# Optimization experiments

Measured on AMD Instinct MI355X. Metric: run time of the kernel, lower is better.

Reference implementation:

```python
import jax, jax.numpy as jnp
import numpy as np

B, N, C, D, K = 8, 4096, 64, 64, 16


def _knn_indices(features, k):
    # so topk-smallest indices match torch.cdist + topk(largest=False))
    sq = jnp.sum(features * features, axis=-1)                      # [B, N]
    d2 = sq[:, :, None] + sq[:, None, :] - 2.0 * jnp.einsum('bic,bjc->bij', features, features)
    n = features.shape[1]
    eye = jnp.eye(n, dtype=bool)[None]                              # mask self
    d2 = jnp.where(eye, jnp.inf, d2)
    _, idx = jax.lax.top_k(-d2, k)                                  # k smallest
    return idx                                                      # [B, N, k]


def setup_inputs() -> dict:
    key = jax.random.key(0)
    k0, k1, k2 = jax.random.split(key, 3)
    features = jax.random.normal(k0, (B, N, C), dtype=jnp.float32)
    W1 = jax.random.normal(k1, (2 * C, D), dtype=jnp.float32) * 0.05
    b1 = jnp.zeros((D,), dtype=jnp.float32)
    W2 = jax.random.normal(k2, (D, D), dtype=jnp.float32) * 0.05
    b2 = jnp.zeros((D,), dtype=jnp.float32)
    return {"features": features, "W1": W1, "b1": b1, "W2": W2, "b2": b2}


def reference(features, W1, b1, W2, b2):
    idx = _knn_indices(features, K)                                 # [B, N, K]
    neighbors = jax.vmap(lambda f, i: f[i])(features, idx)          # [B, N, K, C]
    central = features[:, :, None, :]                               # [B, N, 1, C]
    edge = jnp.concatenate(
        [jnp.broadcast_to(central, neighbors.shape), neighbors - central], axis=-1
    )                                                               # [B, N, K, 2C]
    h = jax.nn.gelu(edge @ W1 + b1, approximate=False)              # exact GELU (torch default)
    h = jax.nn.gelu(h @ W2 + b2, approximate=False)                 # [B, N, K, D]
    return jnp.max(h, axis=2)                                       # [B, N, D]
```

## Files before the change

kernel.cpp:

```cpp
#include <hip/hip_runtime.h>
#include <math.h>
#include <stdint.h>

#define B 8
#define N 4096
#define C 64
#define D 64
#define K 16

typedef __attribute__((ext_vector_type(8))) short short8;
typedef __attribute__((ext_vector_type(4))) float f32x4;

__device__ __forceinline__ unsigned short f2bf(float x) {
    unsigned u = __float_as_uint(x);
    unsigned r = (u + 0x7FFFu + ((u >> 16) & 1u)) >> 16;
    return (unsigned short)r;
}
__device__ __forceinline__ float bf2f(unsigned short h) {
    return __uint_as_float(((unsigned)h) << 16);
}

__device__ __forceinline__ double pack_key(float d2, unsigned idx) {
    uint2 u; u.x = idx; u.y = __float_as_uint(d2);
    return __builtin_bit_cast(double, u);
}

__global__ __launch_bounds__(256)
void prep_kernel(const float* __restrict__ F, float* __restrict__ sq,
                 unsigned short* __restrict__ HP, unsigned short* __restrict__ MP,
                 unsigned short* __restrict__ LP) {
    const int row = blockIdx.x * 256 + threadIdx.x;
    const float4* src = (const float4*)(F + (size_t)row * C);
    float4 v[16];
    #pragma unroll
    for (int q = 0; q < 16; q++) v[q] = src[q];

    {
        float r[8];
        #pragma unroll
        for (int j = 0; j < 8; j++) {
            float t = ((const float*)v)[j];
            r[j] = t * t;
        }
        #pragma unroll
        for (int m = 1; m < 8; m++) {
            #pragma unroll
            for (int j = 0; j < 8; j++) {
                float t = ((const float*)v)[8 * m + j];
                r[j] = fmaf(t, t, r[j]);
            }
        }
        sq[row] = ((r[0] + r[1]) + (r[2] + r[3])) + ((r[4] + r[5]) + (r[6] + r[7]));
    }

    uint4* dh = (uint4*)(HP + (size_t)row * C);
    uint4* dm = (uint4*)(MP + (size_t)row * C);
    uint4* dl = (uint4*)(LP + (size_t)row * C);
    #pragma unroll
    for (int c8 = 0; c8 < 8; c8++) {
        unsigned hq[4], mq[4], lq[4];
        #pragma unroll
        for (int e = 0; e < 4; e++) {
            float x0 = ((const float*)v)[c8 * 8 + 2 * e];
            float x1 = ((const float*)v)[c8 * 8 + 2 * e + 1];
            unsigned short h0 = f2bf(x0), h1 = f2bf(x1);
            float r10 = x0 - bf2f(h0), r11 = x1 - bf2f(h1);
            unsigned short m0 = f2bf(r10), m1 = f2bf(r11);
            float r20 = r10 - bf2f(m0), r21 = r11 - bf2f(m1);
            unsigned short l0 = f2bf(r20), l1 = f2bf(r21);
            hq[e] = (unsigned)h0 | ((unsigned)h1 << 16);
            mq[e] = (unsigned)m0 | ((unsigned)m1 << 16);
            lq[e] = (unsigned)l0 | ((unsigned)l1 << 16);
        }
        dh[c8] = make_uint4(hq[0], hq[1], hq[2], hq[3]);
        dm[c8] = make_uint4(mq[0], mq[1], mq[2], mq[3]);
        dl[c8] = make_uint4(lq[0], lq[1], lq[2], lq[3]);
    }
}

__device__ __forceinline__ void merge4_store(const uint64_t* __restrict__ keys,
                                             int qloc, uint64_t* __restrict__ dst) {
    const uint64_t* K0 = keys + (qloc * 4 + 0) * 16;
    const uint64_t* K1 = keys + (qloc * 4 + 1) * 16;
    const uint64_t* K2 = keys + (qloc * 4 + 2) * 16;
    const uint64_t* K3 = keys + (qloc * 4 + 3) * 16;
    int p0 = 0, p1 = 0, p2 = 0, p3 = 0;
    uint64_t h0 = K0[0], h1 = K1[0], h2 = K2[0], h3 = K3[0];
    #pragma unroll
    for (int k = 0; k < K; k++) {
        uint64_t m01 = h0 < h1 ? h0 : h1;
        uint64_t m23 = h2 < h3 ? h2 : h3;
        uint64_t mv  = m01 < m23 ? m01 : m23;
        dst[k] = mv;
        if      (mv == h0) { ++p0; h0 = (p0 < 16) ? K0[p0] : ~0ull; }
        else if (mv == h1) { ++p1; h1 = (p1 < 16) ? K1[p1] : ~0ull; }
        else if (mv == h2) { ++p2; h2 = (p2 < 16) ? K2[p2] : ~0ull; }
        else               { ++p3; h3 = (p3 < 16) ? K3[p3] : ~0ull; }
    }
}

__global__ __launch_bounds__(512, 2)
void knn_mfma_kernel(const unsigned short* __restrict__ HP,
                     const unsigned short* __restrict__ MP,
                     const unsigned short* __restrict__ LP,
                     const float* __restrict__ sqg, uint64_t* __restrict__ keysg) {
    __shared__ __align__(16) char lds[49152];

    const int s  = blockIdx.y;
    const int b  = blockIdx.z;
    const int i0 = blockIdx.x * 128;
    const int c0 = s * 2048;
    const unsigned short* Hb = HP + (size_t)b * N * C;
    const unsigned short* Mb = MP + (size_t)b * N * C;
    const unsigned short* Lb = LP + (size_t)b * N * C;
    const float* sqb = sqg + (size_t)b * N;

    const int tid = threadIdx.x;
    const int l   = tid & 63;
    const int w   = tid >> 6;

    const int lr  = tid >> 3;
    const int lq  = tid & 7;
    const int wbyte = (lr * 128 + lq * 16) ^ ((lr & 7) << 4);

    const double KMAX = __builtin_bit_cast(double, 0x7FEFFFFFFFFFFFFFull);

    uint4 ph, pm, pl;
    {
        const size_t rb = (size_t)(c0 + lr) * C + lq * 8;
        ph = *(const uint4*)(Hb + rb);
        pm = *(const uint4*)(Mb + rb);
        pl = *(const uint4*)(Lb + rb);
    }

    {
        const size_t r0 = (size_t)(i0 + lr) * C + lq * 8;
        const size_t r1 = (size_t)(i0 + 64 + lr) * C + lq * 8;
        uint4 qh0 = *(const uint4*)(Hb + r0), qh1 = *(const uint4*)(Hb + r1);
        uint4 qm0 = *(const uint4*)(Mb + r0), qm1 = *(const uint4*)(Mb + r1);
        uint4 ql0 = *(const uint4*)(Lb + r0), ql1 = *(const uint4*)(Lb + r1);
        *(uint4*)(lds +              wbyte) = qh0;
        *(uint4*)(lds +  8192      + wbyte) = qm0;
        *(uint4*)(lds + 16384      + wbyte) = ql0;
        *(uint4*)(lds + 24576      + wbyte) = qh1;
        *(uint4*)(lds + 24576+8192 + wbyte) = qm1;
        *(uint4*)(lds + 24576+16384+ wbyte) = ql1;
    }
    __syncthreads();

    const int koff = (l >> 4) * 16;
    const int swzR = (l & 7) << 4;
    const int qrow = w * 16 + (l & 15);
    const char* qbuf = lds + ((qrow >> 6) ? 24576 : 0);
    const int qr6 = qrow & 63;
    const int qb0 = (qr6 * 128 + koff) ^ swzR;
    const int qb1 = (qr6 * 128 + 64 + koff) ^ swzR;
    short8 bh0 = *(const short8*)(qbuf + qb0),         bh1 = *(const short8*)(qbuf + qb1);
    short8 bm0 = *(const short8*)(qbuf +  8192 + qb0), bm1 = *(const short8*)(qbuf +  8192 + qb1);
    short8 bl0 = *(const short8*)(qbuf + 16384 + qb0), bl1 = *(const short8*)(qbuf + 16384 + qb1);

    const float sqq   = sqb[i0 + qrow];
    const int   qglob = i0 + qrow;
    const int   crow0 = (l >> 4) * 4;
    const int   dtile = i0 + ((w >> 2) << 6);

    __syncthreads();

    *(uint4*)(lds +         wbyte) = ph;
    *(uint4*)(lds +  8192 + wbyte) = pm;
    *(uint4*)(lds + 16384 + wbyte) = pl;
    {
        const size_t rb = (size_t)(c0 + 64 + lr) * C + lq * 8;
        ph = *(const uint4*)(Hb + rb);
        pm = *(const uint4*)(Mb + rb);
        pl = *(const uint4*)(Lb + rb);
    }
    __syncthreads();

    double bd[16];
    #pragma unroll
    for (int k = 0; k < 16; k++) bd[k] = KMAX;

    for (int t = 0; t < 32; t++) {
        const int j0 = c0 + t * 64;
        char* bufA = lds + ((t & 1) ? 24576 : 0);
        char* bufB = lds + ((t & 1) ? 0 : 24576);

        if (t < 31) {
            *(uint4*)(bufB +         wbyte) = ph;
            *(uint4*)(bufB +  8192 + wbyte) = pm;
            *(uint4*)(bufB + 16384 + wbyte) = pl;
        }
        if (t < 30) {
            const size_t rb = (size_t)(j0 + 128 + lr) * C + lq * 8;
            ph = *(const uint4*)(Hb + rb);
            pm = *(const uint4*)(Mb + rb);
            pl = *(const uint4*)(Lb + rb);
        }

        float4 sqm0 = *(const float4*)(sqb + j0 +      crow0);
        float4 sqm1 = *(const float4*)(sqb + j0 + 16 + crow0);
        float4 sqm2 = *(const float4*)(sqb + j0 + 32 + crow0);
        float4 sqm3 = *(const float4*)(sqb + j0 + 48 + crow0);

        double nk[16];

        #pragma unroll
        for (int m = 0; m < 4; m++) {
            const int arow = m * 16 + (l & 15);
            const int ab0 = (arow * 128 + koff) ^ swzR;
            const int ab1 = (arow * 128 + 64 + koff) ^ swzR;
            short8 ah0 = *(const short8*)(bufA + ab0);
            short8 ah1 = *(const short8*)(bufA + ab1);
            short8 am0 = *(const short8*)(bufA + 8192 + ab0);
            short8 am1 = *(const short8*)(bufA + 8192 + ab1);
            short8 al0 = *(const short8*)(bufA + 16384 + ab0);
            short8 al1 = *(const short8*)(bufA + 16384 + ab1);

            f32x4 acc1 = {0.f, 0.f, 0.f, 0.f};
            acc1 = __builtin_amdgcn_mfma_f32_16x16x32_bf16(am0, bm0, acc1, 0, 0, 0);
            acc1 = __builtin_amdgcn_mfma_f32_16x16x32_bf16(am1, bm1, acc1, 0, 0, 0);
            acc1 = __builtin_amdgcn_mfma_f32_16x16x32_bf16(ah0, bl0, acc1, 0, 0, 0);
            acc1 = __builtin_amdgcn_mfma_f32_16x16x32_bf16(ah1, bl1, acc1, 0, 0, 0);
            acc1 = __builtin_amdgcn_mfma_f32_16x16x32_bf16(al0, bh0, acc1, 0, 0, 0);
            f32x4 acc2 = {0.f, 0.f, 0.f, 0.f};
            acc2 = __builtin_amdgcn_mfma_f32_16x16x32_bf16(al1, bh1, acc2, 0, 0, 0);
            acc2 = __builtin_amdgcn_mfma_f32_16x16x32_bf16(ah0, bm0, acc2, 0, 0, 0);
            acc2 = __builtin_amdgcn_mfma_f32_16x16x32_bf16(ah1, bm1, acc2, 0, 0, 0);
            acc2 = __builtin_amdgcn_mfma_f32_16x16x32_bf16(am0, bh0, acc2, 0, 0, 0);
            acc2 = __builtin_amdgcn_mfma_f32_16x16x32_bf16(am1, bh1, acc2, 0, 0, 0);
            f32x4 acch = {0.f, 0.f, 0.f, 0.f};
            acch = __builtin_amdgcn_mfma_f32_16x16x32_bf16(ah0, bh0, acch, 0, 0, 0);
            acch = __builtin_amdgcn_mfma_f32_16x16x32_bf16(ah1, bh1, acch, 0, 0, 0);

            float4 sqm = (m == 0) ? sqm0 : (m == 1) ? sqm1 : (m == 2) ? sqm2 : sqm3;
            #pragma unroll
            for (int r = 0; r < 4; r++) {
                float sqc = (r == 0) ? sqm.x : (r == 1) ? sqm.y : (r == 2) ? sqm.z : sqm.w;
                float gg = acch[r] + (acc1[r] + acc2[r]);
                float d2 = fmaf(-2.0f, gg, sqq + sqc);
                d2 = fmaxf(d2, 0.0f);
                nk[m * 4 + r] = pack_key(d2, (unsigned)(j0 + m * 16 + crow0 + r));
            }
        }

        if (j0 == dtile) {
            #pragma unroll
            for (int m = 0; m < 4; m++)
                #pragma unroll
                for (int r = 0; r < 4; r++)
                    if ((j0 + m * 16 + crow0 + r) == qglob) nk[m * 4 + r] = KMAX;
        }

        #pragma unroll
        for (int p = 1; p < 16; p <<= 1) {
            #pragma unroll
            for (int kk = p; kk >= 1; kk >>= 1) {
                #pragma unroll
                for (int j = kk % p; j <= 16 - 1 - kk; j += 2 * kk) {
                    #pragma unroll
                    for (int i = 0; i <= ((kk - 1 < 16 - j - kk - 1) ? kk - 1 : 16 - j - kk - 1); i++) {
                        if ((i + j) / (2 * p) == (i + j + kk) / (2 * p)) {
                            double a = nk[i + j], c2 = nk[i + j + kk];
                            nk[i + j]      = fmax(a, c2);
                            nk[i + j + kk] = fmin(a, c2);
                        }
                    }
                }
            }
        }
        #pragma unroll
        for (int i = 0; i < 16; i++) bd[i] = fmin(bd[i], nk[i]);
        #pragma unroll
        for (int j = 8; j > 0; j >>= 1) {
            #pragma unroll
            for (int i = 0; i < 16; i++) {
                int ixj = i ^ j;
                if (ixj > i) {
                    double a = bd[i], c2 = bd[ixj];
                    bd[i]   = fmin(a, c2);
                    bd[ixj] = fmax(a, c2);
                }
            }
        }

        __syncthreads();
    }

    uint64_t* keys = (uint64_t*)lds;
    if (w < 4) {
        const int qloc = w * 16 + (l & 15);
        const int base = (qloc * 4 + (l >> 4)) * 16;
        #pragma unroll
        for (int k = 0; k < 16; k++)
            keys[base + k] = __builtin_bit_cast(uint64_t, bd[k]);
    }
    __syncthreads();
    if (tid < 64)
        merge4_store(keys, tid, keysg + ((size_t)b * N + i0 + tid) * 32 + s * 16);
    __syncthreads();
    if (w >= 4) {
        const int qloc = (w - 4) * 16 + (l & 15);
        const int base = (qloc * 4 + (l >> 4)) * 16;
        #pragma unroll
        for (int k = 0; k < 16; k++)
            keys[base + k] = __builtin_bit_cast(uint64_t, bd[k]);
    }
    __syncthreads();
    if (tid < 64)
        merge4_store(keys, tid, keysg + ((size_t)b * N + i0 + 64 + tid) * 32 + s * 16);
}

__global__ __launch_bounds__(256)
void knn_merge_kernel(const uint64_t* __restrict__ keysg, int* __restrict__ knn) {
    const int q = blockIdx.x * 256 + threadIdx.x;
    const uint64_t* A  = keysg + (size_t)q * 32;
    const uint64_t* Bp = A + 16;
    int pa = 0, pb = 0;
    uint64_t ha = A[0], hb = Bp[0];
    int* dst = knn + (size_t)q * K;
    #pragma unroll
    for (int k = 0; k < K; k++) {
        uint64_t mv = ha < hb ? ha : hb;
        dst[k] = (int)(mv & 0xFFFFFFFFu);
        if (mv == ha) { ++pa; ha = (pa < 16) ? A[pa] : ~0ull; }
        else          { ++pb; hb = (pb < 16) ? Bp[pb] : ~0ull; }
    }
}

__device__ __forceinline__ float gelu_fast(float x) {
    float az = fabsf(x) * 0.70710678118654752440f;
    float t  = __builtin_amdgcn_rcpf(fmaf(0.3275911f, az, 1.0f));
    float p  = t * fmaf(t, fmaf(t, fmaf(t, fmaf(t, 1.061405429f, -1.453152027f),
                                        1.421413741f), -0.284496736f), 0.254829592f);
    float e  = p * __builtin_amdgcn_exp2f(-az * az * 1.44269504088896f);
    float g  = 0.5f * x;
    return (x >= 0.0f) ? g * (2.0f - e) : g * e;
}

#define QPW 4

__global__ __launch_bounds__(256)
void mlp_mfma_kernel(const float* __restrict__ F,
                     const unsigned short* __restrict__ HP,
                     const unsigned short* __restrict__ MP,
                     const int* __restrict__ knn,
                     const float* __restrict__ W1, const float* __restrict__ b1,
                     const float* __restrict__ W2, const float* __restrict__ b2,
                     float* __restrict__ out) {
    __shared__ __align__(16) unsigned short W1h[64 * 128];
    __shared__ __align__(16) unsigned short W1m[64 * 128];
    __shared__ __align__(16) unsigned short hbh[4][1024];
    __shared__ __align__(16) unsigned short hbm[4][1024];

    const int tid = threadIdx.x;
    const int l   = tid & 63;
    const int w   = tid >> 6;

    const int cb   = (l >> 4) * 8;
    const int swzL = (l & 15) << 4;
    const int qbase = (blockIdx.x * 4 + w) * QPW;

    int nbs[QPW];
    #pragma unroll
    for (int jq = 0; jq < QPW; jq++)
        nbs[jq] = knn[(size_t)(qbase + jq) * K + (l & 15)];

    for (int e = tid; e < 8192; e += 256) {
        const int n = e & 63, k = e >> 6;
        const int srcrow = (k < 64) ? (64 + k) : (k - 64);
        float x = W1[srcrow * 64 + n];
        unsigned short hh = f2bf(x);
        unsigned short mm = f2bf(x - bf2f(hh));
        const int byte = (n * 256 + k * 2) ^ ((n & 15) << 4);
        *(unsigned short*)((char*)W1h + byte) = hh;
        *(unsigned short*)((char*)W1m + byte) = mm;
    }

    short8 B2h[4][2], B2m[4][2];
    float b1v[4], b2v[4];
    {
        const int n = (l & 15);
        #pragma unroll
        for (int nt = 0; nt < 4; nt++) {
            const int nn = nt * 16 + n;
            b1v[nt] = b1[nn];
            b2v[nt] = b2[nn];
            #pragma unroll
            for (int c = 0; c < 2; c++) {
                const int k0 = c * 32 + (l >> 4) * 8;
                short8 vh, vm;
                #pragma unroll
                for (int jj = 0; jj < 8; jj++) {
                    float x = W2[(k0 + jj) * 64 + nn];
                    unsigned short hh = f2bf(x);
                    vh[jj] = (short)hh;
                    vm[jj] = (short)f2bf(x - bf2f(hh));
                }
                B2h[nt][c] = vh; B2m[nt][c] = vm;
            }
        }
    }
    __syncthreads();

    float4 pnA0[2], pnA1[2], pnB0[2], pnB1[2];
    #define LOADN(s_, jq_) { \
        const int q_ = qbase + (jq_); \
        const float* Fb_ = F + (size_t)(q_ >> 12) * N * C; \
        const size_t nr_ = (size_t)nbs[jq_] * C; \
        pnA0[s_] = *(const float4*)(Fb_ + nr_ + cb); \
        pnA1[s_] = *(const float4*)(Fb_ + nr_ + cb + 4); \
        pnB0[s_] = *(const float4*)(Fb_ + nr_ + 32 + cb); \
        pnB1[s_] = *(const float4*)(Fb_ + nr_ + 36 + cb); \
    }
    LOADN(0, 0);

    #pragma unroll
    for (int jq = 0; jq < QPW; jq++) {
        const int sbuf = jq & 1;
        if (jq + 1 < QPW) LOADN(sbuf ^ 1, jq + 1);

        const int q  = qbase + jq;
        const int b  = q >> 12;
        const int ci = q & (N - 1);
        const float*          Fb  = F  + (size_t)b * N * C;
        const unsigned short* HPb = HP + (size_t)b * N * C;
        const unsigned short* MPb = MP + (size_t)b * N * C;

        float4 cA0 = *(const float4*)(Fb + (size_t)ci * C + cb);
        float4 cA1 = *(const float4*)(Fb + (size_t)ci * C + cb + 4);
        float4 cB0 = *(const float4*)(Fb + (size_t)ci * C + 32 + cb);
        float4 cB1 = *(const float4*)(Fb + (size_t)ci * C + 36 + cb);
        float4 nA0 = pnA0[sbuf], nA1 = pnA1[sbuf];
        float4 nB0 = pnB0[sbuf], nB1 = pnB1[sbuf];

        short8 ach0 = *(const short8*)(HPb + (size_t)ci * C + cb);
        short8 ach1 = *(const short8*)(HPb + (size_t)ci * C + 32 + cb);
        short8 acm0 = *(const short8*)(MPb + (size_t)ci * C + cb);
        short8 acm1 = *(const short8*)(MPb + (size_t)ci * C + 32 + cb);

        short8 adh0, adm0, adh1, adm1;
        {
            float d0[8] = {nA0.x - cA0.x, nA0.y - cA0.y, nA0.z - cA0.z, nA0.w - cA0.w,
                           nA1.x - cA1.x, nA1.y - cA1.y, nA1.z - cA1.z, nA1.w - cA1.w};
            float d1[8] = {nB0.x - cB0.x, nB0.y - cB0.y, nB0.z - cB0.z, nB0.w - cB0.w,
                           nB1.x - cB1.x, nB1.y - cB1.y, nB1.z - cB1.z, nB1.w - cB1.w};
            #pragma unroll
            for (int jj = 0; jj < 8; jj++) {
                unsigned short h0 = f2bf(d0[jj]);
                adh0[jj] = (short)h0; adm0[jj] = (short)f2bf(d0[jj] - bf2f(h0));
                unsigned short h1 = f2bf(d1[jj]);
                adh1[jj] = (short)h1; adm1[jj] = (short)f2bf(d1[jj] - bf2f(h1));
            }
        }

        #pragma unroll
        for (int nt = 0; nt < 4; nt++) {
            const int rowb = (nt * 16 + (l & 15)) * 256 + (l >> 4) * 16;
            f32x4 a1 = {0.f, 0.f, 0.f, 0.f};
            f32x4 a2 = {0.f, 0.f, 0.f, 0.f};
            #pragma unroll
            for (int kc = 0; kc < 4; kc++) {
                const int byte = (rowb + kc * 64) ^ swzL;
                short8 Bh = *(const short8*)((char*)W1h + byte);
                short8 Bm = *(const short8*)((char*)W1m + byte);
                short8 Ah = (kc == 0) ? adh0 : (kc == 1) ? adh1 : (kc == 2) ? ach0 : ach1;
                short8 Am = (kc == 0) ? adm0 : (kc == 1) ? adm1 : (kc == 2) ? acm0 : acm1;
                a1 = __builtin_amdgcn_mfma_f32_16x16x32_bf16(Ah, Bh, a1, 0, 0, 0);
                a2 = __builtin_amdgcn_mfma_f32_16x16x32_bf16(Ah, Bm, a2, 0, 0, 0);
                a2 = __builtin_amdgcn_mfma_f32_16x16x32_bf16(Am, Bh, a2, 0, 0, 0);
            }
            #pragma unroll
            for (int r = 0; r < 4; r++) {
                const int row = (l >> 4) * 4 + r;
                const int col = nt * 16 + (l & 15);
                float hv = gelu_fast(a1[r] + a2[r] + b1v[nt]);
                unsigned short hh = f2bf(hv);
                unsigned short hm = f2bf(hv - bf2f(hh));
                const int byte = (row * 128 + col * 2) ^ ((row & 7) << 4);
                *(unsigned short*)((char*)&hbh[w][0] + byte) = hh;
                *(unsigned short*)((char*)&hbm[w][0] + byte) = hm;
            }
        }

        asm volatile("s_waitcnt lgkmcnt(0)" ::: "memory");
        __builtin_amdgcn_sched_barrier(0);

        short8 Ah2[2], Am2[2];
        #pragma unroll
        for (int kc = 0; kc < 2; kc++) {
            const int byte = ((l & 15) * 128 + kc * 64 + (l >> 4) * 16) ^ (((l & 15) & 7) << 4);
            Ah2[kc] = *(const short8*)((char*)&hbh[w][0] + byte);
            Am2[kc] = *(const short8*)((char*)&hbm[w][0] + byte);
        }
        #pragma unroll
        for (int nt = 0; nt < 4; nt++) {
            f32x4 a1 = {0.f, 0.f, 0.f, 0.f};
            f32x4 a2 = {0.f, 0.f, 0.f, 0.f};
            #pragma unroll
            for (int kc = 0; kc < 2; kc++) {
                a1 = __builtin_amdgcn_mfma_f32_16x16x32_bf16(Ah2[kc], B2h[nt][kc], a1, 0, 0, 0);
                a2 = __builtin_amdgcn_mfma_f32_16x16x32_bf16(Ah2[kc], B2m[nt][kc], a2, 0, 0, 0);
                a2 = __builtin_amdgcn_mfma_f32_16x16x32_bf16(Am2[kc], B2h[nt][kc], a2, 0, 0, 0);
            }
            float mx = -INFINITY;
            #pragma unroll
            for (int r = 0; r < 4; r++)
                mx = fmaxf(mx, gelu_fast(a1[r] + a2[r] + b2v[nt]));
            mx = fmaxf(mx, __shfl_xor(mx, 16));
            mx = fmaxf(mx, __shfl_xor(mx, 32));
            if (l < 16) out[(size_t)q * D + nt * 16 + l] = mx;
        }
    }
    #undef LOADN
}

extern "C" void kernel_launch(void* const* d_in, const int* in_sizes, int n_in,
                              void* d_out, int out_size, void* d_ws, size_t ws_size,
                              hipStream_t stream) {
    const float* F  = (const float*)d_in[0];
    const float* W1 = (const float*)d_in[1];
    const float* b1 = (const float*)d_in[2];
    const float* W2 = (const float*)d_in[3];
    const float* b2 = (const float*)d_in[4];
    float* out = (float*)d_out;

    char* ws = (char*)d_ws;
    float*          sq   = (float*)ws;
    uint64_t*       keys = (uint64_t*)(ws + (128 << 10));
    unsigned short* HP   = (unsigned short*)(ws + (8320 << 10));
    unsigned short* MP   = (unsigned short*)(ws + (12416 << 10));
    unsigned short* LP   = (unsigned short*)(ws + (16512 << 10));
    int*            knn  = (int*)LP;

    prep_kernel<<<dim3(B * N / 256), 256, 0, stream>>>(F, sq, HP, MP, LP);
    knn_mfma_kernel<<<dim3(N / 128, 2, B), 512, 0, stream>>>(HP, MP, LP, sq, keys);
    knn_merge_kernel<<<dim3(B * N / 256), 256, 0, stream>>>(keys, knn);
    mlp_mfma_kernel<<<dim3(B * N / (4 * QPW)), 256, 0, stream>>>(
        F, HP, MP, knn, W1, b1, W2, b2, out);
}
```

Before: 267.9 us.

## Precompute split-bf16 weights in prep kernel and software-pipeline MLP layers

The bf16 hi/lo splitting and swizzling of W1 and W2 moves into one block of the prep kernel. Each MLP block now copies the ready-made weights into LDS with vector loads instead of converting them itself, which removes repeated per-block conversion work across 2048 blocks. The MLP loop is also restructured so that layer 1 of the next query is issued before layer 2 of the current one, to overlap MFMA, LDS and global-load latency. In exchange, the single-block weight prep adds a serial tail to the prep kernel and the pipelined loop uses more registers.

```diff
diff --git a/kernel.cpp b/kernel.cpp
--- a/kernel.cpp
+++ b/kernel.cpp
@@ -28,7 +28,10 @@
 __global__ __launch_bounds__(256)
 void prep_kernel(const float* __restrict__ F, float* __restrict__ sq,
                  unsigned short* __restrict__ HP, unsigned short* __restrict__ MP,
-                 unsigned short* __restrict__ LP) {
+                 unsigned short* __restrict__ LP,
+                 const float* __restrict__ W1, const float* __restrict__ W2,
+                 unsigned short* __restrict__ W1hg, unsigned short* __restrict__ W1mg,
+                 unsigned short* __restrict__ W2Th, unsigned short* __restrict__ W2Tm) {
     const int row = blockIdx.x * 256 + threadIdx.x;
     const float4* src = (const float4*)(F + (size_t)row * C);
     float4 v[16];
@@ -75,6 +78,27 @@
         dh[c8] = make_uint4(hq[0], hq[1], hq[2], hq[3]);
         dm[c8] = make_uint4(mq[0], mq[1], mq[2], mq[3]);
         dl[c8] = make_uint4(lq[0], lq[1], lq[2], lq[3]);
+    }
+
+    if (blockIdx.x == 0) {
+        const int tid = threadIdx.x;
+        for (int e = tid; e < 8192; e += 256) {
+            const int n = e & 63, k = e >> 6;
+            const int srcrow = (k < 64) ? (64 + k) : (k - 64);
+            float x = W1[srcrow * 64 + n];
+            unsigned short hh = f2bf(x);
+            unsigned short mm = f2bf(x - bf2f(hh));
+            const int byte = (n * 256 + k * 2) ^ ((n & 15) << 4);
+            *(unsigned short*)((char*)W1hg + byte) = hh;
+            *(unsigned short*)((char*)W1mg + byte) = mm;
+        }
+        for (int e = tid; e < 4096; e += 256) {
+            const int n = e & 63, k = e >> 6;
+            float x = W2[k * 64 + n];
+            unsigned short hh = f2bf(x);
+            W2Th[n * 64 + k] = hh;
+            W2Tm[n * 64 + k] = f2bf(x - bf2f(hh));
+        }
     }
 }
 
@@ -345,8 +369,11 @@
                      const unsigned short* __restrict__ HP,
                      const unsigned short* __restrict__ MP,
                      const int* __restrict__ knn,
-                     const float* __restrict__ W1, const float* __restrict__ b1,
-                     const float* __restrict__ W2, const float* __restrict__ b2,
+                     const unsigned short* __restrict__ W1hg,
+                     const unsigned short* __restrict__ W1mg,
+                     const unsigned short* __restrict__ W2Th,
+                     const unsigned short* __restrict__ W2Tm,
+                     const float* __restrict__ b1, const float* __restrict__ b2,
                      float* __restrict__ out) {
     __shared__ __align__(16) unsigned short W1h[64 * 128];
     __shared__ __align__(16) unsigned short W1m[64 * 128];
@@ -357,54 +384,50 @@
     const int l   = tid & 63;
     const int w   = tid >> 6;
 
-    const int cb   = (l >> 4) * 8;
-    const int swzL = (l & 15) << 4;
+    const int cb    = (l >> 4) * 8;
+    const int swzL  = (l & 15) << 4;
     const int qbase = (blockIdx.x * 4 + w) * QPW;
+    char* hbh_w = (char*)&hbh[w][0];
+    char* hbm_w = (char*)&hbm[w][0];
 
     int nbs[QPW];
     #pragma unroll
     for (int jq = 0; jq < QPW; jq++)
         nbs[jq] = knn[(size_t)(qbase + jq) * K + (l & 15)];
 
-    for (int e = tid; e < 8192; e += 256) {
-        const int n = e & 63, k = e >> 6;
-        const int srcrow = (k < 64) ? (64 + k) : (k - 64);
-        float x = W1[srcrow * 64 + n];
-        unsigned short hh = f2bf(x);
-        unsigned short mm = f2bf(x - bf2f(hh));
-        const int byte = (n * 256 + k * 2) ^ ((n & 15) << 4);
-        *(unsigned short*)((char*)W1h + byte) = hh;
-        *(unsigned short*)((char*)W1m + byte) = mm;
+    {
+        const uint4* s1 = (const uint4*)W1hg;
+        const uint4* s2 = (const uint4*)W1mg;
+        uint4* d1 = (uint4*)W1h;
+        uint4* d2 = (uint4*)W1m;
+        #pragma unroll
+        for (int i = 0; i < 4; i++) {
+            d1[tid + 256 * i] = s1[tid + 256 * i];
+            d2[tid + 256 * i] = s2[tid + 256 * i];
+        }
     }
 
     short8 B2h[4][2], B2m[4][2];
-    float b1v[4], b2v[4];
+    float4 b1v, b2v;
     {
         const int n = (l & 15);
+        b1v = make_float4(b1[n], b1[16 + n], b1[32 + n], b1[48 + n]);
+        b2v = make_float4(b2[n], b2[16 + n], b2[32 + n], b2[48 + n]);
         #pragma unroll
         for (int nt = 0; nt < 4; nt++) {
             const int nn = nt * 16 + n;
-            b1v[nt] = b1[nn];
-            b2v[nt] = b2[nn];
             #pragma unroll
             for (int c = 0; c < 2; c++) {
                 const int k0 = c * 32 + (l >> 4) * 8;
-                short8 vh, vm;
-                #pragma unroll
-                for (int jj = 0; jj < 8; jj++) {
-                    float x = W2[(k0 + jj) * 64 + nn];
-                    unsigned short hh = f2bf(x);
-                    vh[jj] = (short)hh;
-                    vm[jj] = (short)f2bf(x - bf2f(hh));
-                }
-                B2h[nt][c] = vh; B2m[nt][c] = vm;
+                B2h[nt][c] = *(const short8*)(W2Th + nn * 64 + k0);
+                B2m[nt][c] = *(const short8*)(W2Tm + nn * 64 + k0);
             }
         }
     }
     __syncthreads();
 
     float4 pnA0[2], pnA1[2], pnB0[2], pnB1[2];
-    #define LOADN(s_, jq_) { \
+#define LOADN(s_, jq_) { \
         const int q_ = qbase + (jq_); \
         const float* Fb_ = F + (size_t)(q_ >> 12) * N * C; \
         const size_t nr_ = (size_t)nbs[jq_] * C; \
@@ -413,106 +436,125 @@
         pnB0[s_] = *(const float4*)(Fb_ + nr_ + 32 + cb); \
         pnB1[s_] = *(const float4*)(Fb_ + nr_ + 36 + cb); \
     }
+
+#define MLP_L1(jq_) { \
+        const int q_  = qbase + (jq_); \
+        const int b_  = q_ >> 12; \
+        const int ci_ = q_ & (N - 1); \
+        const float*          Fb_  = F  + (size_t)b_ * N * C; \
+        const unsigned short* HPb_ = HP + (size_t)b_ * N * C; \
+        const unsigned short* MPb_ = MP + (size_t)b_ * N * C; \
+        float4 cA0 = *(const float4*)(Fb_ + (size_t)ci_ * C + cb); \
+        float4 cA1 = *(const float4*)(Fb_ + (size_t)ci_ * C + cb + 4); \
+        float4 cB0 = *(const float4*)(Fb_ + (size_t)ci_ * C + 32 + cb); \
+        float4 cB1 = *(const float4*)(Fb_ + (size_t)ci_ * C + 36 + cb); \
+        float4 nA0 = pnA0[(jq_) & 1], nA1 = pnA1[(jq_) & 1]; \
+        float4 nB0 = pnB0[(jq_) & 1], nB1 = pnB1[(jq_) & 1]; \
+        short8 ach0 = *(const short8*)(HPb_ + (size_t)ci_ * C + cb); \
+        short8 ach1 = *(const short8*)(HPb_ + (size_t)ci_ * C + 32 + cb); \
+        short8 acm0 = *(const short8*)(MPb_ + (size_t)ci_ * C + cb); \
+        short8 acm1 = *(const short8*)(MPb_ + (size_t)ci_ * C + 32 + cb); \
+        short8 adh0, adm0, adh1, adm1; \
+        { \
+            float d0[8] = {nA0.x-cA0.x, nA0.y-cA0.y, nA0.z-cA0.z, nA0.w-cA0.w, \
+                           nA1.x-cA1.x, nA1.y-cA1.y, nA1.z-cA1.z, nA1.w-cA1.w}; \
+            float d1[8] = {nB0.x-cB0.x, nB0.y-cB0.y, nB0.z-cB0.z, nB0.w-cB0.w, \
+                           nB1.x-cB1.x, nB1.y-cB1.y, nB1.z-cB1.z, nB1.w-cB1.w}; \
+            _Pragma("unroll") \
+            for (int jj = 0; jj < 8; jj++) { \
+                unsigned short h0_ = f2bf(d0[jj]); \
+                adh0[jj] = (short)h0_; adm0[jj] = (short)f2bf(d0[jj] - bf2f(h0_)); \
+                unsigned short h1_ = f2bf(d1[jj]); \
+                adh1[jj] = (short)h1_; adm1[jj] = (short)f2bf(d1[jj] - bf2f(h1_)); \
+            } \
+        } \
+        _Pragma("unroll") \
+        for (int nt = 0; nt < 4; nt++) { \
+            const int rowb = (nt * 16 + (l & 15)) * 256 + (l >> 4) * 16; \
+            f32x4 a1 = {0.f,0.f,0.f,0.f}; \
+            f32x4 a2 = {0.f,0.f,0.f,0.f}; \
+            _Pragma("unroll") \
+            for (int kc = 0; kc < 4; kc++) { \
+                const int byte_ = (rowb + kc * 64) ^ swzL; \
+                short8 Bh = *(const short8*)((char*)W1h + byte_); \
+                short8 Bm = *(const short8*)((char*)W1m + byte_); \
+                short8 Ah = (kc==0)?adh0:(kc==1)?adh1:(kc==2)?ach0:ach1; \
+                short8 Am = (kc==0)?adm0:(kc==1)?adm1:(kc==2)?acm0:acm1; \
+                a1 = __builtin_amdgcn_mfma_f32_16x16x32_bf16(Ah, Bh, a1, 0, 0, 0); \
+                a2 = __builtin_amdgcn_mfma_f32_16x16x32_bf16(Ah, Bm, a2, 0, 0, 0); \
+                a2 = __builtin_amdgcn_mfma_f32_16x16x32_bf16(Am, Bh, a2, 0, 0, 0); \
+            } \
+            float bnt = (nt==0)?b1v.x:(nt==1)?b1v.y:(nt==2)?b1v.z:b1v.w; \
+            _Pragma("unroll") \
+            for (int r = 0; r < 4; r++) { \
+                const int row = (l >> 4) * 4 + r; \
+                const int col = nt * 16 + (l & 15); \
+                float hv = gelu_fast(a1[r] + a2[r] + bnt); \
+                unsigned short hh_ = f2bf(hv); \
+                unsigned short hm_ = f2bf(hv - bf2f(hh_)); \
+                const int byte_ = (row * 128 + col * 2) ^ ((row & 7) << 4); \
+                *(unsigned short*)(hbh_w + byte_) = hh_; \
+                *(unsigned short*)(hbm_w + byte_) = hm_; \
+            } \
+        } \
+    }
+
+#define WAITREAD() { \
+        asm volatile("s_waitcnt lgkmcnt(0)" ::: "memory"); \
+        __builtin_amdgcn_sched_barrier(0); \
+        _Pragma("unroll") \
+        for (int kc = 0; kc < 2; kc++) { \
+            const int byte_ = ((l & 15) * 128 + kc * 64 + (l >> 4) * 16) ^ (((l & 15) & 7) << 4); \
+            A2h[kc] = *(const short8*)(hbh_w + byte_); \
+            A2m[kc] = *(const short8*)(hbm_w + byte_); \
+        } \
+    }
+
+#define MLP_L2(jq_) { \
+        const int q_ = qbase + (jq_); \
+        _Pragma("unroll") \
+        for (int nt = 0; nt < 4; nt++) { \
+            f32x4 a1 = {0.f,0.f,0.f,0.f}; \
+            f32x4 a2 = {0.f,0.f,0.f,0.f}; \
+            _Pragma("unroll") \
+            for (int kc = 0; kc < 2; kc++) { \
+                a1 = __builtin_amdgcn_mfma_f32_16x16x32_bf16(A2h[kc], B2h[nt][kc], a1, 0, 0, 0); \
+                a2 = __builtin_amdgcn_mfma_f32_16x16x32_bf16(A2h[kc], B2m[nt][kc], a2, 0, 0, 0); \
+                a2 = __builtin_amdgcn_mfma_f32_16x16x32_bf16(A2m[kc], B2h[nt][kc], a2, 0, 0, 0); \
+            } \
+            float bnt = (nt==0)?b2v.x:(nt==1)?b2v.y:(nt==2)?b2v.z:b2v.w; \
+            float mx = -INFINITY; \
+            _Pragma("unroll") \
+            for (int r = 0; r < 4; r++) \
+                mx = fmaxf(mx, gelu_fast(a1[r] + a2[r] + bnt)); \
+            mx = fmaxf(mx, __shfl_xor(mx, 16)); \
+            mx = fmaxf(mx, __shfl_xor(mx, 32)); \
+            if (l < 16) out[(size_t)q_ * D + nt * 16 + l] = mx; \
+        } \
+    }
+
+    short8 A2h[2], A2m[2];
+
     LOADN(0, 0);
+    LOADN(1, 1);
+    MLP_L1(0);
+    WAITREAD();
 
     #pragma unroll
     for (int jq = 0; jq < QPW; jq++) {
-        const int sbuf = jq & 1;
-        if (jq + 1 < QPW) LOADN(sbuf ^ 1, jq + 1);
-
-        const int q  = qbase + jq;
-        const int b  = q >> 12;
-        const int ci = q & (N - 1);
-        const float*          Fb  = F  + (size_t)b * N * C;
-        const unsigned short* HPb = HP + (size_t)b * N * C;
-        const unsigned short* MPb = MP + (size_t)b * N * C;
-
-        float4 cA0 = *(const float4*)(Fb + (size_t)ci * C + cb);
-        float4 cA1 = *(const float4*)(Fb + (size_t)ci * C + cb + 4);
-        float4 cB0 = *(const float4*)(Fb + (size_t)ci * C + 32 + cb);
-        float4 cB1 = *(const float4*)(Fb + (size_t)ci * C + 36 + cb);
-        float4 nA0 = pnA0[sbuf], nA1 = pnA1[sbuf];
-        float4 nB0 = pnB0[sbuf], nB1 = pnB1[sbuf];
-
-        short8 ach0 = *(const short8*)(HPb + (size_t)ci * C + cb);
-        short8 ach1 = *(const short8*)(HPb + (size_t)ci * C + 32 + cb);
-        short8 acm0 = *(const short8*)(MPb + (size_t)ci * C + cb);
-        short8 acm1 = *(const short8*)(MPb + (size_t)ci * C + 32 + cb);
-
-        short8 adh0, adm0, adh1, adm1;
-        {
-            float d0[8] = {nA0.x - cA0.x, nA0.y - cA0.y, nA0.z - cA0.z, nA0.w - cA0.w,
-                           nA1.x - cA1.x, nA1.y - cA1.y, nA1.z - cA1.z, nA1.w - cA1.w};
-            float d1[8] = {nB0.x - cB0.x, nB0.y - cB0.y, nB0.z - cB0.z, nB0.w - cB0.w,
-                           nB1.x - cB1.x, nB1.y - cB1.y, nB1.z - cB1.z, nB1.w - cB1.w};
-            #pragma unroll
-            for (int jj = 0; jj < 8; jj++) {
-                unsigned short h0 = f2bf(d0[jj]);
-                adh0[jj] = (short)h0; adm0[jj] = (short)f2bf(d0[jj] - bf2f(h0));
-                unsigned short h1 = f2bf(d1[jj]);
-                adh1[jj] = (short)h1; adm1[jj] = (short)f2bf(d1[jj] - bf2f(h1));
-            }
-        }
-
-        #pragma unroll
-        for (int nt = 0; nt < 4; nt++) {
-            const int rowb = (nt * 16 + (l & 15)) * 256 + (l >> 4) * 16;
-            f32x4 a1 = {0.f, 0.f, 0.f, 0.f};
-            f32x4 a2 = {0.f, 0.f, 0.f, 0.f};
-            #pragma unroll
-            for (int kc = 0; kc < 4; kc++) {
-                const int byte = (rowb + kc * 64) ^ swzL;
-                short8 Bh = *(const short8*)((char*)W1h + byte);
-                short8 Bm = *(const short8*)((char*)W1m + byte);
-                short8 Ah = (kc == 0) ? adh0 : (kc == 1) ? adh1 : (kc == 2) ? ach0 : ach1;
-                short8 Am = (kc == 0) ? adm0 : (kc == 1) ? adm1 : (kc == 2) ? acm0 : acm1;
-                a1 = __builtin_amdgcn_mfma_f32_16x16x32_bf16(Ah, Bh, a1, 0, 0, 0);
-                a2 = __builtin_amdgcn_mfma_f32_16x16x32_bf16(Ah, Bm, a2, 0, 0, 0);
-                a2 = __builtin_amdgcn_mfma_f32_16x16x32_bf16(Am, Bh, a2, 0, 0, 0);
-            }
-            #pragma unroll
-            for (int r = 0; r < 4; r++) {
-                const int row = (l >> 4) * 4 + r;
-                const int col = nt * 16 + (l & 15);
-                float hv = gelu_fast(a1[r] + a2[r] + b1v[nt]);
-                unsigned short hh = f2bf(hv);
-                unsigned short hm = f2bf(hv - bf2f(hh));
-                const int byte = (row * 128 + col * 2) ^ ((row & 7) << 4);
-                *(unsigned short*)((char*)&hbh[w][0] + byte) = hh;
-                *(unsigned short*)((char*)&hbm[w][0] + byte) = hm;
-            }
-        }
-
-        asm volatile("s_waitcnt lgkmcnt(0)" ::: "memory");
-        __builtin_amdgcn_sched_barrier(0);
-
-        short8 Ah2[2], Am2[2];
-        #pragma unroll
-        for (int kc = 0; kc < 2; kc++) {
-            const int byte = ((l & 15) * 128 + kc * 64 + (l >> 4) * 16) ^ (((l & 15) & 7) << 4);
-            Ah2[kc] = *(const short8*)((char*)&hbh[w][0] + byte);
-            Am2[kc] = *(const short8*)((char*)&hbm[w][0] + byte);
-        }
-        #pragma unroll
-        for (int nt = 0; nt < 4; nt++) {
-            f32x4 a1 = {0.f, 0.f, 0.f, 0.f};
-            f32x4 a2 = {0.f, 0.f, 0.f, 0.f};
-            #pragma unroll
-            for (int kc = 0; kc < 2; kc++) {
-                a1 = __builtin_amdgcn_mfma_f32_16x16x32_bf16(Ah2[kc], B2h[nt][kc], a1, 0, 0, 0);
-                a2 = __builtin_amdgcn_mfma_f32_16x16x32_bf16(Ah2[kc], B2m[nt][kc], a2, 0, 0, 0);
-                a2 = __builtin_amdgcn_mfma_f32_16x16x32_bf16(Am2[kc], B2h[nt][kc], a2, 0, 0, 0);
-            }
-            float mx = -INFINITY;
-            #pragma unroll
-            for (int r = 0; r < 4; r++)
-                mx = fmaxf(mx, gelu_fast(a1[r] + a2[r] + b2v[nt]));
-            mx = fmaxf(mx, __shfl_xor(mx, 16));
-            mx = fmaxf(mx, __shfl_xor(mx, 32));
-            if (l < 16) out[(size_t)q * D + nt * 16 + l] = mx;
-        }
-    }
-    #undef LOADN
+        if (jq + 1 < QPW) {
+            MLP_L1(jq + 1);
+        }
+        MLP_L2(jq);
+        if (jq + 1 < QPW) {
+            if (jq + 2 < QPW) LOADN((jq + 2) & 1, jq + 2);
+            WAITREAD();
+        }
+    }
+#undef LOADN
+#undef MLP_L1
+#undef WAITREAD
+#undef MLP_L2
 }
 
 extern "C" void kernel_launch(void* const* d_in, const int* in_sizes, int n_in,
@@ -531,11 +573,16 @@
     unsigned short* HP   = (unsigned short*)(ws + (8320 << 10));
     unsigned short* MP   = (unsigned short*)(ws + (12416 << 10));
     unsigned short* LP   = (unsigned short*)(ws + (16512 << 10));
+    unsigned short* W1hg = (unsigned short*)(ws + (20608 << 10));
+    unsigned short* W1mg = (unsigned short*)(ws + (20624 << 10));
+    unsigned short* W2Th = (unsigned short*)(ws + (20640 << 10));
+    unsigned short* W2Tm = (unsigned short*)(ws + (20648 << 10));
     int*            knn  = (int*)LP;
 
-    prep_kernel<<<dim3(B * N / 256), 256, 0, stream>>>(F, sq, HP, MP, LP);
+    prep_kernel<<<dim3(B * N / 256), 256, 0, stream>>>(F, sq, HP, MP, LP,
+                                                       W1, W2, W1hg, W1mg, W2Th, W2Tm);
     knn_mfma_kernel<<<dim3(N / 128, 2, B), 512, 0, stream>>>(HP, MP, LP, sq, keys);
     knn_merge_kernel<<<dim3(B * N / 256), 256, 0, stream>>>(keys, knn);
     mlp_mfma_kernel<<<dim3(B * N / (4 * QPW)), 256, 0, stream>>>(
-        F, HP, MP, knn, W1, b1, W2, b2, out);
-}
+        F, HP, MP, knn, W1hg, W1mg, W2Th, W2Tm, b1, b2, out);
+}
```

After: 277.5 us. 3.6% more time.
